# Kernel optimization log

Hardware: AMD Instinct MI355X
Metric: run time of the kernel (lower is better)

The kernel has to match this reference:

```python
import jax, jax.numpy as jnp
import numpy as np

B, D_IN, D_OUT, Q, NUM_CLASSES = 256, 512, 256, 16, 100
POOL = 2  # patch_size = sqrt(n=4) -> 2x2 spatial mean pooling


def setup_inputs() -> dict:
    key = jax.random.key(0)
    k1, k2, k3 = jax.random.split(key, 3)
    X = jax.random.normal(k1, (B, D_IN, Q), jnp.float32)
    # FRMap weight init: randn(d_out, d_in) / sqrt(d_in)
    W = jax.random.normal(k2, (D_OUT, D_IN), jnp.float32) / np.sqrt(D_IN)
    d2 = D_OUT // POOL
    fc_w = jax.random.normal(k3, (NUM_CLASSES, d2 * d2), jnp.float32) / np.sqrt(d2 * d2)
    fc_b = jnp.zeros((NUM_CLASSES,), jnp.float32)
    return {"X": X, "W": W, "fc_w": fc_w, "fc_b": fc_b}


def reference(X, W, fc_w, fc_b):
    # FRMap: Y = W @ X  -> (B, d_out, q)
    Y = jnp.einsum('oi,biq->boq', W, X)
    # ReOrth: Q from reduced QR of Y -> orthonormal (B, d_out, q)
    Qm, _ = jnp.linalg.qr(Y)
    # ProjMap: P = Q Q^T -> (B, d_out, d_out)
    P = jnp.einsum('biq,bjq->bij', Qm, Qm)
    # ProjPooling (spatial, n=4): 2x2 mean pooling == adaptive_avg_pool2d to (d/2, d/2)
    b, d, _ = P.shape
    d2 = d // POOL
    Pp = P.reshape(b, d2, POOL, d2, POOL).mean(axis=(2, 4))  # (B, d2, d2)
    # OrthMap: top-q eigenvectors of symmetric Pp (eigh ascending -> take last q, descending)
    _, V = jnp.linalg.eigh(Pp)
    U = V[..., ::-1][..., :Q]  # (B, d2, q)
    # OutputBlock: ProjMap + flatten + FC
    P2 = jnp.einsum('biq,bjq->bij', U, U)  # (B, d2, d2)
    logits = P2.reshape(b, -1) @ fc_w.T + fc_b  # (B, num_classes)
    return logits
```

## Files before the change

kernel.cpp:

```cpp
#include <hip/hip_runtime.h>
#include <hip/hip_bf16.h>
#include <cstdint>

#define BATCH 256
#define DIN   512
#define D2    128
#define NQ    16
#define NC    100
#define KFC   (D2 * D2)

#define KS    32
#define KCH   (KFC / KS)
#define STEPS (KCH / 32)

#define ZPAD  132
#define CVT_BLKS 800
#define W2_BLKS  256

typedef short short8 __attribute__((ext_vector_type(8)));
typedef float f32x4  __attribute__((ext_vector_type(4)));
typedef float f32x16 __attribute__((ext_vector_type(16)));

static __device__ __forceinline__ unsigned short f2bf_rne(float f) {
    unsigned x = __float_as_uint(f);
    return (unsigned short)((x + 0x7fffu + ((x >> 16) & 1u)) >> 16);
}
static __device__ __forceinline__ float bf2f(unsigned short u) {
    return __uint_as_float(((unsigned)u) << 16);
}

__global__ __launch_bounds__(256) void k_prep(const float* __restrict__ W,
                                              const float* __restrict__ fcw,
                                              __hip_bfloat16* __restrict__ W2hi,
                                              __hip_bfloat16* __restrict__ W2lo,
                                              __hip_bfloat16* __restrict__ fcw16) {
    int blk = blockIdx.x;
    if (blk < CVT_BLKS) {
        int i = (blk * 256 + threadIdx.x) * 8;
        float4 a = *(const float4*)(fcw + i);
        float4 b = *(const float4*)(fcw + i + 4);
        short8 v;
        unsigned short* h = (unsigned short*)&v;
        h[0] = f2bf_rne(a.x); h[1] = f2bf_rne(a.y);
        h[2] = f2bf_rne(a.z); h[3] = f2bf_rne(a.w);
        h[4] = f2bf_rne(b.x); h[5] = f2bf_rne(b.y);
        h[6] = f2bf_rne(b.z); h[7] = f2bf_rne(b.w);
        *(short8*)(fcw16 + i) = v;
    } else {
        int idx = (blk - CVT_BLKS) * 256 + threadIdx.x;
        int o = idx >> 9;
        int i = idx & (DIN - 1);
        float v = 0.5f * (W[(size_t)(2 * o) * DIN + i] +
                          W[(size_t)(2 * o + 1) * DIN + i]);
        unsigned short hi = f2bf_rne(v);
        unsigned short lo = f2bf_rne(v - bf2f(hi));
        *(unsigned short*)(W2hi + idx) = hi;
        *(unsigned short*)(W2lo + idx) = lo;
    }
}

#define GJ_STEP(K) do {                                                   \
    float piv = __shfl(g[(K) & 7], ((K) >> 3) * 16 + (K), 64);            \
    float fac = __shfl(g[(K) & 7], ((K) >> 3) * 16 + r, 64);              \
    float inv = 1.0f / piv;                                               \
    float f   = fac * inv;                                                \
    float p0 = __shfl(g[0], cg16 + (K), 64);                              \
    float p1 = __shfl(g[1], cg16 + (K), 64);                              \
    float p2 = __shfl(g[2], cg16 + (K), 64);                              \
    float p3 = __shfl(g[3], cg16 + (K), 64);                              \
    float p4 = __shfl(g[4], cg16 + (K), 64);                              \
    float p5 = __shfl(g[5], cg16 + (K), 64);                              \
    float p6 = __shfl(g[6], cg16 + (K), 64);                              \
    float p7 = __shfl(g[7], cg16 + (K), 64);                              \
    bool isk = (r == (K));                                                \
    g[0] = isk ? p0 * inv : fmaf(-f, p0, g[0]);                           \
    g[1] = isk ? p1 * inv : fmaf(-f, p1, g[1]);                           \
    g[2] = isk ? p2 * inv : fmaf(-f, p2, g[2]);                           \
    g[3] = isk ? p3 * inv : fmaf(-f, p3, g[3]);                           \
    g[4] = isk ? p4 * inv : fmaf(-f, p4, g[4]);                           \
    g[5] = isk ? p5 * inv : fmaf(-f, p5, g[5]);                           \
    g[6] = isk ? p6 * inv : fmaf(-f, p6, g[6]);                           \
    g[7] = isk ? p7 * inv : fmaf(-f, p7, g[7]);                           \
} while (0)

__global__ __launch_bounds__(512) void k_zgep(const float* __restrict__ X,
                                              const __hip_bfloat16* __restrict__ W2hi,
                                              const __hip_bfloat16* __restrict__ W2lo,
                                              __hip_bfloat16* __restrict__ P2) {
    __shared__ float Xs[DIN][17];
    __shared__ unsigned int FragHi[16 * 256];
    __shared__ unsigned int FragLo[16 * 256];
    __shared__ float Zt[NQ][ZPAD];
    __shared__ float Et[NQ][ZPAD];
    __shared__ float Gi[NQ][36];

    int b = blockIdx.x;
    int t = threadIdx.x;
    int l = t & 63;
    int wv = t >> 6;

    {
        const float4* src = (const float4*)(X + (size_t)b * DIN * NQ);
        #pragma unroll
        for (int r = 0; r < 4; ++r) {
            float4 v = src[t + r * 512];
            int idx = (t + r * 512) * 4;
            int i = idx >> 4, q = idx & 15;
            Xs[i][q]     = v.x;
            Xs[i][q + 1] = v.y;
            Xs[i][q + 2] = v.z;
            Xs[i][q + 3] = v.w;
        }
    }
    __syncthreads();

    #pragma unroll
    for (int it = 0; it < 8; ++it) {
        int d  = t + it * 512;
        int s  = d >> 8;
        int ln = (d >> 2) & 63;
        int jj = d & 3;
        int q  = ln & 15;
        int i0 = s * 32 + ((ln >> 4) & 3) * 8 + jj * 2;
        float v0 = Xs[i0][q], v1 = Xs[i0 + 1][q];
        unsigned short h0 = f2bf_rne(v0), h1 = f2bf_rne(v1);
        unsigned short l0 = f2bf_rne(v0 - bf2f(h0));
        unsigned short l1 = f2bf_rne(v1 - bf2f(h1));
        FragHi[d] = (unsigned)h0 | ((unsigned)h1 << 16);
        FragLo[d] = (unsigned)l0 | ((unsigned)l1 << 16);
    }
    __syncthreads();

    {
        int m  = l & 15;
        int kg = (l >> 4) * 8;
        const __hip_bfloat16* whi = W2hi + (size_t)(wv * 16 + m) * DIN + kg;
        const __hip_bfloat16* wlo = W2lo + (size_t)(wv * 16 + m) * DIN + kg;
        f32x4 acc = {0.f, 0.f, 0.f, 0.f};
        #pragma unroll 4
        for (int s = 0; s < 16; ++s) {
            short8 ahi = *(const short8*)(whi + s * 32);
            short8 alo = *(const short8*)(wlo + s * 32);
            short8 bhi = *(const short8*)(&FragHi[s * 256 + l * 4]);
            short8 blo = *(const short8*)(&FragLo[s * 256 + l * 4]);
            acc = __builtin_amdgcn_mfma_f32_16x16x32_bf16(ahi, bhi, acc, 0, 0, 0);
            acc = __builtin_amdgcn_mfma_f32_16x16x32_bf16(ahi, blo, acc, 0, 0, 0);
            acc = __builtin_amdgcn_mfma_f32_16x16x32_bf16(alo, bhi, acc, 0, 0, 0);
        }
        int r0 = (l >> 4) * 4;
        #pragma unroll
        for (int j = 0; j < 4; ++j)
            Zt[m][wv * 16 + r0 + j] = acc[j];
    }
    __syncthreads();

    if (t < 256) {
        int qq = t >> 4, rr = t & 15;
        float s = 0.f;
        for (int i = 0; i < D2; i += 4) {
            float4 a = *(const float4*)&Zt[qq][i];
            float4 c = *(const float4*)&Zt[rr][i];
            s = fmaf(a.x, c.x, s); s = fmaf(a.y, c.y, s);
            s = fmaf(a.z, c.z, s); s = fmaf(a.w, c.w, s);
        }
        Gi[qq][rr] = s;
        Gi[qq][NQ + rr] = (qq == rr) ? 1.f : 0.f;
    }
    __syncthreads();

    if (t < 64) {
        int r    = t & 15;
        int cgg  = t >> 4;
        int cg16 = cgg * 16;
        float g[8];
        #pragma unroll
        for (int j = 0; j < 8; ++j) g[j] = Gi[r][cgg * 8 + j];
        GJ_STEP(0);  GJ_STEP(1);  GJ_STEP(2);  GJ_STEP(3);
        GJ_STEP(4);  GJ_STEP(5);  GJ_STEP(6);  GJ_STEP(7);
        GJ_STEP(8);  GJ_STEP(9);  GJ_STEP(10); GJ_STEP(11);
        GJ_STEP(12); GJ_STEP(13); GJ_STEP(14); GJ_STEP(15);
        if (cgg >= 2) {
            #pragma unroll
            for (int j = 0; j < 8; ++j) Gi[r][cgg * 8 + j] = g[j];
        }
    }
    __syncthreads();

    {
        int o  = t & (D2 - 1);
        int qg = (t >> 7) * 4;
        float acc[4] = {};
        #pragma unroll
        for (int rp = 0; rp < NQ; ++rp) {
            float z = Zt[rp][o];
            #pragma unroll
            for (int j = 0; j < 4; ++j)
                acc[j] = fmaf(z, Gi[rp][NQ + qg + j], acc[j]);
        }
        #pragma unroll
        for (int j = 0; j < 4; ++j) Et[qg + j][o] = acc[j];
    }
    __syncthreads();

    {
        __hip_bfloat16* P2b = P2 + (size_t)b * KFC;
        int ti = wv >> 1;
        int tj0 = (wv & 1) * 2;
        int r8 = (l >> 5) * 8;
        int rm = l & 31;

        short8 afr;
        {
            unsigned short* ah = (unsigned short*)&afr;
            #pragma unroll
            for (int j = 0; j < 8; ++j)
                ah[j] = f2bf_rne(Et[r8 + j][ti * 32 + rm]);
        }
        #pragma unroll
        for (int tjo = 0; tjo < 2; ++tjo) {
            int tj = tj0 + tjo;
            short8 bfr;
            unsigned short* bh = (unsigned short*)&bfr;
            #pragma unroll
            for (int j = 0; j < 8; ++j)
                bh[j] = f2bf_rne(Zt[r8 + j][tj * 32 + rm]);
            f32x16 cc = {};
            cc = __builtin_amdgcn_mfma_f32_32x32x16_bf16(afr, bfr, cc, 0, 0, 0);
            #pragma unroll
            for (int reg = 0; reg < 16; ++reg) {
                int row = (reg & 3) + 8 * (reg >> 2) + 4 * (l >> 5);
                P2b[(size_t)(ti * 32 + row) * D2 + tj * 32 + rm] =
                    __float2bfloat16(cc[reg]);
            }
        }
    }
}

__global__ __launch_bounds__(256) void k_fc(const __hip_bfloat16* __restrict__ P2,
                                            const __hip_bfloat16* __restrict__ fcw16,
                                            float* __restrict__ part) {
    int bt = blockIdx.x;
    int ks = blockIdx.y;
    int t  = threadIdx.x;
    int lane = t & 63;
    int w    = t >> 6;
    int m  = lane & 15;
    int kg = (lane >> 4) * 8;

    const __hip_bfloat16* pa =
        P2 + (size_t)(bt * 16 + m) * KFC + ks * KCH + kg;

    int c0 = w * 32 + m;
    int c1 = c0 + 16;
    bool v0 = (c0 < NC), v1 = (c1 < NC);
    const __hip_bfloat16* pb0 =
        fcw16 + (size_t)(v0 ? c0 : 0) * KFC + ks * KCH + kg;
    const __hip_bfloat16* pb1 =
        fcw16 + (size_t)(v1 ? c1 : 0) * KFC + ks * KCH + kg;

    f32x4 acc0 = {0.f, 0.f, 0.f, 0.f};
    f32x4 acc1 = {0.f, 0.f, 0.f, 0.f};
    short8 zz = {};

    #pragma unroll 4
    for (int s = 0; s < STEPS; ++s) {
        short8 a  = *(const short8*)(pa + s * 32);
        short8 b0 = v0 ? *(const short8*)(pb0 + s * 32) : zz;
        short8 b1 = v1 ? *(const short8*)(pb1 + s * 32) : zz;
        acc0 = __builtin_amdgcn_mfma_f32_16x16x32_bf16(a, b0, acc0, 0, 0, 0);
        acc1 = __builtin_amdgcn_mfma_f32_16x16x32_bf16(a, b1, acc1, 0, 0, 0);
    }

    int r0 = (lane >> 4) * 4;
    float* pp = part + ((size_t)ks * BATCH + bt * 16 + r0) * D2;
    #pragma unroll
    for (int j = 0; j < 4; ++j) {
        pp[(size_t)j * D2 + w * 32 + m]      = acc0[j];
        pp[(size_t)j * D2 + w * 32 + 16 + m] = acc1[j];
    }
}

__global__ __launch_bounds__(128) void k_red(const float* __restrict__ part,
                                             const float* __restrict__ fcb,
                                             float* __restrict__ out) {
    int b = blockIdx.x;
    int c = threadIdx.x;
    if (c < NC) {
        float s = fcb[c];
        #pragma unroll 8
        for (int ks = 0; ks < KS; ++ks)
            s += part[((size_t)ks * BATCH + b) * D2 + c];
        out[(size_t)b * NC + c] = s;
    }
}

extern "C" void kernel_launch(void* const* d_in, const int* in_sizes, int n_in,
                              void* d_out, int out_size, void* d_ws, size_t ws_size,
                              hipStream_t stream) {
    const float* X   = (const float*)d_in[0];
    const float* W   = (const float*)d_in[1];
    const float* fcw = (const float*)d_in[2];
    const float* fcb = (const float*)d_in[3];
    float* out = (float*)d_out;

    __hip_bfloat16* W2hi  = (__hip_bfloat16*)d_ws;
    __hip_bfloat16* W2lo  = W2hi + 65536;
    __hip_bfloat16* fcw16 = W2lo + 65536;
    __hip_bfloat16* P2b16 = fcw16 + 1638400;
    float*          part  = (float*)(P2b16 + 4194304);

    k_prep<<<dim3(CVT_BLKS + W2_BLKS), 256, 0, stream>>>(W, fcw, W2hi, W2lo, fcw16);
    k_zgep<<<dim3(BATCH), 512, 0, stream>>>(X, W2hi, W2lo, P2b16);
    k_fc  <<<dim3(16, KS), 256, 0, stream>>>(P2b16, fcw16, part);
    k_red <<<dim3(BATCH), 128, 0, stream>>>(part, fcb, out);
}
```

Baseline: 41.91 us.

## Fuse FC split-K partials and reduction into one kernel with LDS reduce

Replaces the split-K FC GEMM (32 K-slices writing partials to global memory) and the separate reduction kernel with one kernel. Each block handles 16 batch rows by 16 classes, and eight waves each cover a 2048-wide K slice before being summed in shared memory together with the bias. This drops one launch and the global round trip of the partial sums. In exchange the grid is only 112 blocks, and each wave runs a longer serial MFMA loop, which may leave the GPU underused.

```diff
diff --git a/kernel.cpp b/kernel.cpp
--- a/kernel.cpp
+++ b/kernel.cpp
@@ -8,10 +8,6 @@
 #define NQ    16
 #define NC    100
 #define KFC   (D2 * D2)
-
-#define KS    32
-#define KCH   (KFC / KS)
-#define STEPS (KCH / 32)
 
 #define ZPAD  132
 #define CVT_BLKS 800
@@ -236,61 +232,48 @@
     }
 }
 
-__global__ __launch_bounds__(256) void k_fc(const __hip_bfloat16* __restrict__ P2,
-                                            const __hip_bfloat16* __restrict__ fcw16,
-                                            float* __restrict__ part) {
-    int bt = blockIdx.x;
-    int ks = blockIdx.y;
-    int t  = threadIdx.x;
-    int lane = t & 63;
-    int w    = t >> 6;
-    int m  = lane & 15;
-    int kg = (lane >> 4) * 8;
-
-    const __hip_bfloat16* pa =
-        P2 + (size_t)(bt * 16 + m) * KFC + ks * KCH + kg;
-
-    int c0 = w * 32 + m;
-    int c1 = c0 + 16;
-    bool v0 = (c0 < NC), v1 = (c1 < NC);
-    const __hip_bfloat16* pb0 =
-        fcw16 + (size_t)(v0 ? c0 : 0) * KFC + ks * KCH + kg;
-    const __hip_bfloat16* pb1 =
-        fcw16 + (size_t)(v1 ? c1 : 0) * KFC + ks * KCH + kg;
-
-    f32x4 acc0 = {0.f, 0.f, 0.f, 0.f};
-    f32x4 acc1 = {0.f, 0.f, 0.f, 0.f};
-    short8 zz = {};
-
-    #pragma unroll 4
-    for (int s = 0; s < STEPS; ++s) {
-        short8 a  = *(const short8*)(pa + s * 32);
-        short8 b0 = v0 ? *(const short8*)(pb0 + s * 32) : zz;
-        short8 b1 = v1 ? *(const short8*)(pb1 + s * 32) : zz;
-        acc0 = __builtin_amdgcn_mfma_f32_16x16x32_bf16(a, b0, acc0, 0, 0, 0);
-        acc1 = __builtin_amdgcn_mfma_f32_16x16x32_bf16(a, b1, acc1, 0, 0, 0);
-    }
-
-    int r0 = (lane >> 4) * 4;
-    float* pp = part + ((size_t)ks * BATCH + bt * 16 + r0) * D2;
-    #pragma unroll
-    for (int j = 0; j < 4; ++j) {
-        pp[(size_t)j * D2 + w * 32 + m]      = acc0[j];
-        pp[(size_t)j * D2 + w * 32 + 16 + m] = acc1[j];
-    }
-}
-
-__global__ __launch_bounds__(128) void k_red(const float* __restrict__ part,
+__global__ __launch_bounds__(512) void k_fc3(const __hip_bfloat16* __restrict__ P2,
+                                             const __hip_bfloat16* __restrict__ fcw16,
                                              const float* __restrict__ fcb,
                                              float* __restrict__ out) {
-    int b = blockIdx.x;
-    int c = threadIdx.x;
-    if (c < NC) {
-        float s = fcb[c];
-        #pragma unroll 8
-        for (int ks = 0; ks < KS; ++ks)
-            s += part[((size_t)ks * BATCH + b) * D2 + c];
-        out[(size_t)b * NC + c] = s;
+    __shared__ float Ls[8][64][5];
+
+    int bt = blockIdx.x;
+    int ct = blockIdx.y;
+    int t  = threadIdx.x;
+    int l  = t & 63;
+    int w  = t >> 6;
+    int m  = l & 15;
+    int kg = (l >> 4) * 8;
+
+    const __hip_bfloat16* pa =
+        P2 + (size_t)(bt * 16 + m) * KFC + w * 2048 + kg;
+    int c = ct * 16 + m;
+    const __hip_bfloat16* pb =
+        fcw16 + (size_t)(c < NC ? c : 0) * KFC + w * 2048 + kg;
+
+    f32x4 acc = {0.f, 0.f, 0.f, 0.f};
+    #pragma unroll 4
+    for (int s = 0; s < 64; ++s) {
+        short8 a = *(const short8*)(pa + s * 32);
+        short8 b = *(const short8*)(pb + s * 32);
+        acc = __builtin_amdgcn_mfma_f32_16x16x32_bf16(a, b, acc, 0, 0, 0);
+    }
+    #pragma unroll
+    for (int j = 0; j < 4; ++j) Ls[w][l][j] = acc[j];
+    __syncthreads();
+
+    if (t < 256) {
+        int ll = t & 63;
+        int j  = t >> 6;
+        float s = Ls[0][ll][j];
+        #pragma unroll
+        for (int ww = 1; ww < 8; ++ww) s += Ls[ww][ll][j];
+        int row = (ll >> 4) * 4 + j;
+        int col = ll & 15;
+        int cc  = ct * 16 + col;
+        if (cc < NC)
+            out[(size_t)(bt * 16 + row) * NC + cc] = s + fcb[cc];
     }
 }
 
@@ -307,10 +290,8 @@
     __hip_bfloat16* W2lo  = W2hi + 65536;
     __hip_bfloat16* fcw16 = W2lo + 65536;
     __hip_bfloat16* P2b16 = fcw16 + 1638400;
-    float*          part  = (float*)(P2b16 + 4194304);
 
     k_prep<<<dim3(CVT_BLKS + W2_BLKS), 256, 0, stream>>>(W, fcw, W2hi, W2lo, fcw16);
     k_zgep<<<dim3(BATCH), 512, 0, stream>>>(X, W2hi, W2lo, P2b16);
-    k_fc  <<<dim3(16, KS), 256, 0, stream>>>(P2b16, fcw16, part);
-    k_red <<<dim3(BATCH), 128, 0, stream>>>(part, fcb, out);
-}
+    k_fc3 <<<dim3(16, 7), 512, 0, stream>>>(P2b16, fcw16, fcb, out);
+}
```

Result: slower. 57.67 us (+37.6%).
